# Performance work log

Hardware: AMD Instinct MI355X
Metric: run time of the kernel (lower is better)

## Reference

```python
import jax, jax.numpy as jnp
import numpy as np

NUM_HEADS = 16
HEAD_DIM = 32  # dim=512 / num_heads=16


def _rel_pos_bias(table, index, window_area):
    # table: [(2W-1)^2, H], index: [N, N] int -> bias [1, H, N, N]
    bias = table[index.reshape(-1)].reshape(window_area, window_area, -1)
    return jnp.transpose(bias, (2, 0, 1))[None]


def setup_inputs() -> dict:
    key = jax.random.key(0)
    ks = jax.random.split(key, 6)
    B, N, C = 256, 196, 512
    x = jax.random.normal(ks[0], (B, N, C), dtype=jnp.float32)
    qkv_w = jax.random.normal(ks[1], (3 * C, C), dtype=jnp.float32) * 0.02
    proj_w = jax.random.normal(ks[2], (C, C), dtype=jnp.float32) * 0.02
    proj_b = jax.random.normal(ks[3], (C,), dtype=jnp.float32) * 0.02
    rel_pos_bias_table = jax.random.normal(ks[4], (729, NUM_HEADS), dtype=jnp.float32) * 0.02
    rel_pos_index = jax.random.randint(ks[5], (N, N), 0, 729, dtype=jnp.int64)
    return {
        "x": x,
        "qkv_w": qkv_w,
        "proj_w": proj_w,
        "proj_b": proj_b,
        "rel_pos_bias_table": rel_pos_bias_table,
        "rel_pos_index": rel_pos_index,
        "window_area": N,
    }


def reference(x, qkv_w, proj_w, proj_b, rel_pos_bias_table, rel_pos_index, window_area):
    B, N, C = x.shape
    H, hd = NUM_HEADS, HEAD_DIM
    scale = hd ** -0.5
    # qkv projection (no bias), split into q,k,v: [B, H, N, hd]
    qkv = (x @ qkv_w.T).reshape(B, N, 3, H, hd)
    qkv = jnp.transpose(qkv, (2, 0, 3, 1, 4))
    q, k, v = qkv[0], qkv[1], qkv[2]
    attn = jnp.einsum("bhnd,bhmd->bhnm", q * scale, k)
    attn = attn + _rel_pos_bias(rel_pos_bias_table, rel_pos_index, window_area)
    attn = jax.nn.softmax(attn, axis=-1)
    out = jnp.einsum("bhnm,bhmd->bhnd", attn, v)
    out = jnp.transpose(out, (0, 2, 1, 3)).reshape(B, N, C)
    return out @ proj_w.T + proj_b
```

## Files before the change

### kernel.cpp

```cpp
#include <hip/hip_runtime.h>
#include <hip/hip_bf16.h>


typedef unsigned short u16;
typedef unsigned int u32;
typedef __attribute__((ext_vector_type(8))) short bf16x8;
typedef __attribute__((ext_vector_type(4))) float f32x4;

#define AS1 __attribute__((address_space(1)))
#define AS3 __attribute__((address_space(3)))

__device__ __forceinline__ u16 f2bf(float f) {
  union { float f; unsigned u; } c; c.f = f;
  unsigned r = ((c.u >> 16) & 1u) + 0x7fffu;
  return (u16)((c.u + r) >> 16);
}

__global__ __launch_bounds__(256) void cvt_f32_bf16(const float* __restrict__ in,
                                                    u16* __restrict__ out, int n) {
  int i = (blockIdx.x * 256 + threadIdx.x) * 4;
  if (i >= n) return;
  float4 v = *(const float4*)(in + i);
  ushort4 o;
  o.x = f2bf(v.x); o.y = f2bf(v.y); o.z = f2bf(v.z); o.w = f2bf(v.w);
  *(ushort4*)(out + i) = o;
}

__global__ __launch_bounds__(256) void zero_vt_pad(u16* __restrict__ vt) {
  int i = blockIdx.x * 256 + threadIdx.x;
  if (i >= 4096 * 32 * 36) return;
  int row = i / 36, c = i - row * 36;
  vt[row * 232 + 196 + c] = 0;
}

__global__ __launch_bounds__(256) void build_bias(const float* __restrict__ table,
                                                  const int* __restrict__ idx,
                                                  u16* __restrict__ outb) {
  int e = blockIdx.x * 256 + threadIdx.x;
  int r = e & 3, lane = (e >> 2) & 63, rest = e >> 8;
  int mt = rest % 14; rest /= 14;
  int nt = rest % 13; int h = rest / 13;
  int n = nt * 16 + (lane & 15);
  int m = mt * 16 + ((lane >> 4) << 2) + r;
  float v;
  if (m < 196) {
    int nc = n < 196 ? n : 195;
    v = table[idx[nc * 196 + m] * 16 + h];
  } else {
    v = -1e30f;
  }
  outb[e] = f2bf(v);
}

template<int KT>
__device__ __forceinline__ void ktile(u16* __restrict__ SMEM,
    const u16* __restrict__ gA0, const u16* __restrict__ gA1,
    const u16* __restrict__ gB0, const u16* __restrict__ gB1,
    int wbase, int rdA, int rdB, f32x4 (&acc)[8][4]) {
  constexpr int BUF = KT & 1, OBUF = BUF ^ 1;
  constexpr bool STG = (KT < 7);
  constexpr int C = (KT + 1) * 64;
  bf16x8 afr[4], bfr[4];

#define LOADPAIR(dst, g0, g1, coloff)                                          \
  __builtin_amdgcn_global_load_lds((const AS1 void*)((g0) + (coloff)),         \
      (AS3 void*)&SMEM[(dst) + wbase], 16, 0, 0);                              \
  __builtin_amdgcn_global_load_lds((const AS1 void*)((g1) + (coloff)),         \
      (AS3 void*)&SMEM[(dst) + 4096 + wbase], 16, 0, 0);
#define MFMA16(FH)                                                             \
  __builtin_amdgcn_s_setprio(1);                                               \
  _Pragma("unroll") for (int q = 0; q < 4; ++q)                                \
    _Pragma("unroll") for (int j = 0; j < 4; ++j)                              \
      acc[(FH)*4 + q][j] = __builtin_amdgcn_mfma_f32_16x16x32_bf16(            \
          afr[q], bfr[j], acc[(FH)*4 + q][j], 0, 0, 0);                        \
  __builtin_amdgcn_s_setprio(0);

#pragma unroll
  for (int j = 0; j < 4; ++j) bfr[j] = *(const bf16x8*)&SMEM[rdB + BUF * 16384 + j * 512];
#pragma unroll
  for (int q = 0; q < 4; ++q) afr[q] = *(const bf16x8*)&SMEM[rdA + BUF * 16384 + q * 512];
  if constexpr (STG) { LOADPAIR(OBUF * 16384, gA0, gA1, C) }
  __builtin_amdgcn_s_barrier();
  asm volatile("s_waitcnt lgkmcnt(0)" ::: "memory");
  MFMA16(0)
  __builtin_amdgcn_s_barrier();
#pragma unroll
  for (int q = 0; q < 4; ++q) afr[q] = *(const bf16x8*)&SMEM[rdA + BUF * 16384 + (q + 4) * 512];
  if constexpr (STG) { LOADPAIR(32768 + OBUF * 16384, gB0, gB1, C) }
  __builtin_amdgcn_s_barrier();
  asm volatile("s_waitcnt lgkmcnt(0)" ::: "memory");
  MFMA16(1)
  if constexpr (STG) { asm volatile("s_waitcnt vmcnt(4)" ::: "memory"); }
  else               { asm volatile("s_waitcnt vmcnt(0)" ::: "memory"); }
  __builtin_amdgcn_s_barrier();
#pragma unroll
  for (int j = 0; j < 4; ++j) bfr[j] = *(const bf16x8*)&SMEM[rdB + BUF * 16384 + 8192 + j * 512];
#pragma unroll
  for (int q = 0; q < 4; ++q) afr[q] = *(const bf16x8*)&SMEM[rdA + BUF * 16384 + 8192 + q * 512];
  if constexpr (STG) { LOADPAIR(OBUF * 16384 + 8192, gA0, gA1, C + 32) }
  __builtin_amdgcn_s_barrier();
  asm volatile("s_waitcnt lgkmcnt(0)" ::: "memory");
  MFMA16(0)
  __builtin_amdgcn_s_barrier();
#pragma unroll
  for (int q = 0; q < 4; ++q) afr[q] = *(const bf16x8*)&SMEM[rdA + BUF * 16384 + 8192 + (q + 4) * 512];
  if constexpr (STG) { LOADPAIR(32768 + OBUF * 16384 + 8192, gB0, gB1, C + 32) }
  __builtin_amdgcn_s_barrier();
  asm volatile("s_waitcnt lgkmcnt(0)" ::: "memory");
  MFMA16(1)
  if constexpr (STG) { asm volatile("s_waitcnt vmcnt(4)" ::: "memory"); }
  __builtin_amdgcn_s_barrier();
#undef LOADPAIR
#undef MFMA16
}

template<int EPI>
__global__ __launch_bounds__(512, 2) void gemm8p(
    const u16* __restrict__ A, const u16* __restrict__ Bt,
    u16* __restrict__ q, u16* __restrict__ kk, u16* __restrict__ vt,
    const float* __restrict__ pbias, float* __restrict__ out) {
  constexpr int NWGX = (EPI == 0) ? 6 : 2;
  constexpr int NWG = NWGX * 196;
  __shared__ __align__(16) u16 SMEM[65536];

  int id = blockIdx.y * NWGX + blockIdx.x;
  int nf = (id & 7) * (NWG >> 3) + (id >> 3);
  const int bx = nf / NWGX, by = nf - (nf / NWGX) * NWGX;

  const int tid = threadIdx.x;
  const int w = tid >> 6, l = tid & 63;
  const int lr = l & 15, lg = l >> 4;
  const int wm = w >> 2, wn = w & 3;

  const int gsw = (l & 3) ^ ((l >> 3) & 3);
  const u16* gA0 = A + (size_t)(bx * 256 + w * 16 + (l >> 2)) * 512 + gsw * 8;
  const u16* gA1 = gA0 + 65536;
  const u16* gB0 = Bt + (size_t)(by * 256 + w * 16 + (l >> 2)) * 512 + gsw * 8;
  const u16* gB1 = gB0 + 65536;
  const int wbase = w * 512;

  const int rsw = (lg ^ ((lr >> 1) & 3)) * 8;
  const int rdA = (wm * 128 + lr) * 32 + rsw;
  const int rdB = 32768 + (wn * 64 + lr) * 32 + rsw;

  f32x4 acc[8][4] = {};

#define PLP(dst, g0, g1, coloff)                                               \
  __builtin_amdgcn_global_load_lds((const AS1 void*)((g0) + (coloff)),         \
      (AS3 void*)&SMEM[(dst) + wbase], 16, 0, 0);                              \
  __builtin_amdgcn_global_load_lds((const AS1 void*)((g1) + (coloff)),         \
      (AS3 void*)&SMEM[(dst) + 4096 + wbase], 16, 0, 0);
  PLP(0, gA0, gA1, 0)
  asm volatile("" ::: "memory");
  PLP(32768, gB0, gB1, 0)
  asm volatile("" ::: "memory");
  PLP(8192, gA0, gA1, 32)
  asm volatile("" ::: "memory");
  PLP(32768 + 8192, gB0, gB1, 32)
#undef PLP
  asm volatile("s_waitcnt vmcnt(4)" ::: "memory");
  __builtin_amdgcn_s_barrier();

  ktile<0>(SMEM, gA0, gA1, gB0, gB1, wbase, rdA, rdB, acc);
  ktile<1>(SMEM, gA0, gA1, gB0, gB1, wbase, rdA, rdB, acc);
  ktile<2>(SMEM, gA0, gA1, gB0, gB1, wbase, rdA, rdB, acc);
  ktile<3>(SMEM, gA0, gA1, gB0, gB1, wbase, rdA, rdB, acc);
  ktile<4>(SMEM, gA0, gA1, gB0, gB1, wbase, rdA, rdB, acc);
  ktile<5>(SMEM, gA0, gA1, gB0, gB1, wbase, rdA, rdB, acc);
  ktile<6>(SMEM, gA0, gA1, gB0, gB1, wbase, rdA, rdB, acc);
  ktile<7>(SMEM, gA0, gA1, gB0, gB1, wbase, rdA, rdB, acc);

  if (EPI == 0) {
    const int t = by >> 1;
    const int colbase = by * 256;
    const float s = (t == 0) ? 0.17677669529663687f : 1.0f;
#pragma unroll
    for (int p = 0; p < 2; ++p) {
      __syncthreads();
      if (wm == p) {
        if (t < 2) {
#pragma unroll
        for (int f = 0; f < 8; ++f)
#pragma unroll
          for (int j2 = 0; j2 < 4; ++j2)
#pragma unroll
            for (int r = 0; r < 4; ++r)
              SMEM[(f * 16 + lg * 4 + r) * 264 + wn * 64 + j2 * 16 + lr] =
                  f2bf(acc[f][j2][r] * s);
        } else {
#pragma unroll
        for (int f = 0; f < 8; ++f)
#pragma unroll
          for (int j2 = 0; j2 < 4; ++j2)
#pragma unroll
            for (int r = 0; r < 4; ++r)
              SMEM[(wn * 64 + j2 * 16 + lr) * 136 + f * 16 + lg * 4 + r] =
                  f2bf(acc[f][j2][r]);
        }
      }
      __syncthreads();
      const int growbase = bx * 256 + p * 128;
      if (t < 2) {
        u16* dst = (t == 0) ? q : kk;
        const int lrow = tid >> 2, ch = tid & 3;
        const int grow = growbase + lrow;
        const int bb2 = grow / 196, nn = grow - bb2 * 196;
#pragma unroll
        for (int i = 0; i < 8; ++i) {
          const int colle = (ch + i * 4) * 8;
          bf16x8 vv = *(const bf16x8*)&SMEM[lrow * 264 + colle];
          const int col = colbase + colle;
          const int h = (col >> 5) & 15, dd = col & 31;
          *(bf16x8*)&dst[((size_t)(bb2 * 16 + h) * 196 + nn) * 32 + dd] = vv;
        }
      } else {
        const int cl = tid >> 1, half = tid & 1;
        const int col = colbase + cl;
        const int h = (col >> 5) & 15, dd = col & 31;
#pragma unroll
        for (int i = 0; i < 8; ++i) {
          const int r0 = growbase + half * 64 + i * 8;
          bf16x8 vv = *(const bf16x8*)&SMEM[cl * 136 + half * 64 + i * 8];
          const int bb2 = r0 / 196, nn = r0 - bb2 * 196;
          if (nn + 8 <= 196) {
            *(bf16x8*)&vt[((size_t)(bb2 * 16 + h) * 32 + dd) * 232 + nn] = vv;
          } else {
#pragma unroll
            for (int e = 0; e < 8; ++e) {
              const int rr = r0 + e;
              const int b3 = rr / 196, n3 = rr - b3 * 196;
              vt[((size_t)(b3 * 16 + h) * 32 + dd) * 232 + n3] = (u16)((short*)&vv)[e];
            }
          }
        }
      }
    }
  } else {
    const int colbase = by * 256 + wn * 64;
    const int rowb = bx * 256 + wm * 128 + lg * 4;
#pragma unroll
    for (int f = 0; f < 8; ++f) {
      const int row0 = rowb + f * 16;
#pragma unroll
      for (int j2 = 0; j2 < 4; ++j2) {
        const int col = colbase + j2 * 16 + lr;
        const float pb = pbias[col];
#pragma unroll
        for (int r = 0; r < 4; ++r)
          out[(size_t)(row0 + r) * 512 + col] = acc[f][j2][r] + pb;
      }
    }
  }
}

__global__ __launch_bounds__(256, 4) void attn_kernel(
    const u16* __restrict__ q, const u16* __restrict__ kk,
    const u16* __restrict__ vt, const u16* __restrict__ biasA,
    u16* __restrict__ ao) {
  __shared__ u16 Ks[196 * 40];
  __shared__ u16 Vs[32 * 232];
  const int bhd = blockIdx.x;
  const int h = bhd >> 8, bb = bhd & 255;
  const int bh = bb * 16 + h;
  const int tid = threadIdx.x, w = tid >> 6, l = tid & 63;
  const int lr = l & 15, lg = l >> 4;

  {
    const u16* kg = kk + (size_t)bh * (196 * 32);
#pragma unroll
    for (int p = 0; p < 4; ++p) {
      int m = p * 64 + (tid >> 2);
      if (m < 196) {
        int c = (tid & 3) * 8;
        *(bf16x8*)&Ks[m * 40 + c] = *(const bf16x8*)(kg + m * 32 + c);
      }
    }
    const u16* vg = vt + (size_t)bh * (32 * 232);
#pragma unroll
    for (int p = 0; p < 4; ++p) {
      int off = (p * 256 + tid) * 8;
      if (off < 32 * 232) *(bf16x8*)&Vs[off] = *(const bf16x8*)(vg + off);
    }
  }
  __syncthreads();

  const u16* biasH = biasA + (size_t)h * (13 * 14 * 256);
  const int sA = ((l & 16) << 1) + lr;
  const int sB = sA + 16;
  const bool hi = (l & 32) != 0;

  for (int nt = w; nt < 13; nt += 4) {
    int nq = nt * 16 + lr; if (nq > 195) nq = 195;
    bf16x8 qa = *(const bf16x8*)(q + ((size_t)bh * 196 + nq) * 32 + lg * 8);

    u32 pk[14][2];
    float ssum = 0.f;
#pragma unroll
    for (int mt = 0; mt < 14; ++mt) {
      int row = mt * 16 + lr; if (row > 195) row = 195;
      bf16x8 kb = *(const bf16x8*)&Ks[row * 40 + lg * 8];
      const ushort4 b4 = *(const ushort4*)(biasH + ((nt * 14 + mt) * 64 + l) * 4);
      f32x4 c;
      c[0] = __uint_as_float(((u32)b4.x) << 16);
      c[1] = __uint_as_float(((u32)b4.y) << 16);
      c[2] = __uint_as_float(((u32)b4.z) << 16);
      c[3] = __uint_as_float(((u32)b4.w) << 16);
      f32x4 S = __builtin_amdgcn_mfma_f32_16x16x32_bf16(kb, qa, c, 0, 0, 0);
      float e0 = __expf(S[0]), e1 = __expf(S[1]);
      float e2 = __expf(S[2]), e3 = __expf(S[3]);
      ssum += (e0 + e1) + (e2 + e3);
      asm("v_cvt_pk_bf16_f32 %0, %1, %2" : "=v"(pk[mt][0]) : "v"(e0), "v"(e1));
      asm("v_cvt_pk_bf16_f32 %0, %1, %2" : "=v"(pk[mt][1]) : "v"(e2), "v"(e3));
    }
    ssum += __shfl_xor(ssum, 16);
    ssum += __shfl_xor(ssum, 32);
    float invT = __builtin_amdgcn_rcpf(ssum);

    f32x4 O0 = {}, O1 = {};
#pragma unroll
    for (int ks = 0; ks < 7; ++ks) {
      u32 a0 = (u32)__shfl((int)pk[2 * ks][0], sA);
      u32 a1 = (u32)__shfl((int)pk[2 * ks][1], sA);
      u32 a2 = (u32)__shfl((int)pk[2 * ks][0], sB);
      u32 a3 = (u32)__shfl((int)pk[2 * ks][1], sB);
      u32 c0 = (u32)__shfl((int)pk[2 * ks + 1][0], sA);
      u32 c1 = (u32)__shfl((int)pk[2 * ks + 1][1], sA);
      u32 c2 = (u32)__shfl((int)pk[2 * ks + 1][0], sB);
      u32 c3 = (u32)__shfl((int)pk[2 * ks + 1][1], sB);
      bf16x8 pa;
      ((u32*)&pa)[0] = hi ? c0 : a0;
      ((u32*)&pa)[1] = hi ? c1 : a1;
      ((u32*)&pa)[2] = hi ? c2 : a2;
      ((u32*)&pa)[3] = hi ? c3 : a3;
      bf16x8 v0 = *(const bf16x8*)&Vs[lr * 232 + ks * 32 + lg * 8];
      bf16x8 v1 = *(const bf16x8*)&Vs[(16 + lr) * 232 + ks * 32 + lg * 8];
      O0 = __builtin_amdgcn_mfma_f32_16x16x32_bf16(pa, v0, O0, 0, 0, 0);
      O1 = __builtin_amdgcn_mfma_f32_16x16x32_bf16(pa, v1, O1, 0, 0, 0);
    }

    float inv[4];
#pragma unroll
    for (int r = 0; r < 4; ++r) inv[r] = __shfl(invT, lg * 4 + r);
    const int nr0 = nt * 16 + lg * 4;
#pragma unroll
    for (int r = 0; r < 4; ++r) {
      int nr = nr0 + r;
      if (nr < 196) {
        size_t base = ((size_t)bb * 196 + nr) * 512 + h * 32;
        ao[base + lr] = f2bf(O0[r] * inv[r]);
        ao[base + 16 + lr] = f2bf(O1[r] * inv[r]);
      }
    }
  }
}

extern "C" void kernel_launch(void* const* d_in, const int* in_sizes, int n_in,
                              void* d_out, int out_size, void* d_ws, size_t ws_size,
                              hipStream_t stream) {
  const float* x      = (const float*)d_in[0];
  const float* qkv_w  = (const float*)d_in[1];
  const float* proj_w = (const float*)d_in[2];
  const float* proj_b = (const float*)d_in[3];
  const float* table  = (const float*)d_in[4];
  const int*   ridx   = (const int*)d_in[5];
  float* out = (float*)d_out;

  char* ws = (char*)d_ws;
  u16*   xb    = (u16*)(ws);
  u16*   qwb   = (u16*)(ws + 51380224);
  u16*   pwb   = (u16*)(ws + 52953088);
  u16*   qb    = (u16*)(ws + 53477376);
  u16*   kb    = (u16*)(ws + 104857600);
  u16*   vtb   = (u16*)(ws + 156237824);
  u16*   biasA = (u16*)(ws + 217055232);

  cvt_f32_bf16<<<25088, 256, 0, stream>>>(x, xb, 25690112);
  cvt_f32_bf16<<<768, 256, 0, stream>>>(qkv_w, qwb, 786432);
  cvt_f32_bf16<<<256, 256, 0, stream>>>(proj_w, pwb, 262144);
  build_bias<<<2912, 256, 0, stream>>>(table, ridx, biasA);
  zero_vt_pad<<<18432, 256, 0, stream>>>(vtb);

  gemm8p<0><<<dim3(6, 196), 512, 0, stream>>>(xb, qwb, qb, kb, vtb, nullptr, nullptr);
  attn_kernel<<<4096, 256, 0, stream>>>(qb, kb, vtb, biasA, xb );
  gemm8p<1><<<dim3(2, 196), 512, 0, stream>>>(xb, pwb, nullptr, nullptr, nullptr, proj_b, out);
}
```

Baseline: 273.7 us.

## Hoist K/V fragments into registers, interleave QK and PV, drop pad kernel

The attention kernel now loads all K and V MFMA fragments from shared memory into registers once per block instead of once per query tile. QK^T and PV are interleaved per pair of key tiles, so the 14-entry probability buffer is no longer live. The V padding columns beyond 196 are zeroed in registers, which removes the separate zero_vt_pad launch. Occupancy hint drops from 4 to 3 blocks per SIMD to make room for the larger register footprint, which risks lower latency hiding.

After: 338.5 us. 1.24x slower.

```diff
diff --git a/kernel.cpp b/kernel.cpp
--- a/kernel.cpp
+++ b/kernel.cpp
@@ -24,13 +24,6 @@
   ushort4 o;
   o.x = f2bf(v.x); o.y = f2bf(v.y); o.z = f2bf(v.z); o.w = f2bf(v.w);
   *(ushort4*)(out + i) = o;
-}
-
-__global__ __launch_bounds__(256) void zero_vt_pad(u16* __restrict__ vt) {
-  int i = blockIdx.x * 256 + threadIdx.x;
-  if (i >= 4096 * 32 * 36) return;
-  int row = i / 36, c = i - row * 36;
-  vt[row * 232 + 196 + c] = 0;
 }
 
 __global__ __launch_bounds__(256) void build_bias(const float* __restrict__ table,
@@ -253,7 +246,7 @@
   }
 }
 
-__global__ __launch_bounds__(256, 4) void attn_kernel(
+__global__ __launch_bounds__(256, 3) void attn_kernel(
     const u16* __restrict__ q, const u16* __restrict__ kk,
     const u16* __restrict__ vt, const u16* __restrict__ biasA,
     u16* __restrict__ ao) {
@@ -284,6 +277,27 @@
   }
   __syncthreads();
 
+  bf16x8 kb[14], va[7], vb[7];
+#pragma unroll
+  for (int mt = 0; mt < 14; ++mt) {
+    int row = mt * 16 + lr; if (row > 195) row = 195;
+    kb[mt] = *(const bf16x8*)&Ks[row * 40 + lg * 8];
+  }
+#pragma unroll
+  for (int ks = 0; ks < 7; ++ks) {
+    va[ks] = *(const bf16x8*)&Vs[lr * 232 + ks * 32 + lg * 8];
+    vb[ks] = *(const bf16x8*)&Vs[(16 + lr) * 232 + ks * 32 + lg * 8];
+  }
+  {
+    bf16x8 z = {};
+    if (lg == 0) {
+      va[6][4] = 0; va[6][5] = 0; va[6][6] = 0; va[6][7] = 0;
+      vb[6][4] = 0; vb[6][5] = 0; vb[6][6] = 0; vb[6][7] = 0;
+    } else {
+      va[6] = z; vb[6] = z;
+    }
+  }
+
   const u16* biasH = biasA + (size_t)h * (13 * 14 * 256);
   const int sA = ((l & 16) << 1) + lr;
   const int sB = sA + 16;
@@ -292,51 +306,62 @@
   for (int nt = w; nt < 13; nt += 4) {
     int nq = nt * 16 + lr; if (nq > 195) nq = 195;
     bf16x8 qa = *(const bf16x8*)(q + ((size_t)bh * 196 + nq) * 32 + lg * 8);
-
-    u32 pk[14][2];
     float ssum = 0.f;
-#pragma unroll
-    for (int mt = 0; mt < 14; ++mt) {
-      int row = mt * 16 + lr; if (row > 195) row = 195;
-      bf16x8 kb = *(const bf16x8*)&Ks[row * 40 + lg * 8];
-      const ushort4 b4 = *(const ushort4*)(biasH + ((nt * 14 + mt) * 64 + l) * 4);
-      f32x4 c;
-      c[0] = __uint_as_float(((u32)b4.x) << 16);
-      c[1] = __uint_as_float(((u32)b4.y) << 16);
-      c[2] = __uint_as_float(((u32)b4.z) << 16);
-      c[3] = __uint_as_float(((u32)b4.w) << 16);
-      f32x4 S = __builtin_amdgcn_mfma_f32_16x16x32_bf16(kb, qa, c, 0, 0, 0);
-      float e0 = __expf(S[0]), e1 = __expf(S[1]);
-      float e2 = __expf(S[2]), e3 = __expf(S[3]);
-      ssum += (e0 + e1) + (e2 + e3);
-      asm("v_cvt_pk_bf16_f32 %0, %1, %2" : "=v"(pk[mt][0]) : "v"(e0), "v"(e1));
-      asm("v_cvt_pk_bf16_f32 %0, %1, %2" : "=v"(pk[mt][1]) : "v"(e2), "v"(e3));
-    }
-    ssum += __shfl_xor(ssum, 16);
-    ssum += __shfl_xor(ssum, 32);
-    float invT = __builtin_amdgcn_rcpf(ssum);
-
     f32x4 O0 = {}, O1 = {};
+
 #pragma unroll
     for (int ks = 0; ks < 7; ++ks) {
-      u32 a0 = (u32)__shfl((int)pk[2 * ks][0], sA);
-      u32 a1 = (u32)__shfl((int)pk[2 * ks][1], sA);
-      u32 a2 = (u32)__shfl((int)pk[2 * ks][0], sB);
-      u32 a3 = (u32)__shfl((int)pk[2 * ks][1], sB);
-      u32 c0 = (u32)__shfl((int)pk[2 * ks + 1][0], sA);
-      u32 c1 = (u32)__shfl((int)pk[2 * ks + 1][1], sA);
-      u32 c2 = (u32)__shfl((int)pk[2 * ks + 1][0], sB);
-      u32 c3 = (u32)__shfl((int)pk[2 * ks + 1][1], sB);
+      u32 pk0, pk1, pk2, pk3;
+      {
+        const int mt = 2 * ks;
+        const ushort4 b4 = *(const ushort4*)(biasH + ((nt * 14 + mt) * 64 + l) * 4);
+        f32x4 c;
+        c[0] = __uint_as_float(((u32)b4.x) << 16);
+        c[1] = __uint_as_float(((u32)b4.y) << 16);
+        c[2] = __uint_as_float(((u32)b4.z) << 16);
+        c[3] = __uint_as_float(((u32)b4.w) << 16);
+        f32x4 S = __builtin_amdgcn_mfma_f32_16x16x32_bf16(kb[mt], qa, c, 0, 0, 0);
+        float e0 = __expf(S[0]), e1 = __expf(S[1]);
+        float e2 = __expf(S[2]), e3 = __expf(S[3]);
+        ssum += (e0 + e1) + (e2 + e3);
+        asm("v_cvt_pk_bf16_f32 %0, %1, %2" : "=v"(pk0) : "v"(e0), "v"(e1));
+        asm("v_cvt_pk_bf16_f32 %0, %1, %2" : "=v"(pk1) : "v"(e2), "v"(e3));
+      }
+      {
+        const int mt = 2 * ks + 1;
+        const ushort4 b4 = *(const ushort4*)(biasH + ((nt * 14 + mt) * 64 + l) * 4);
+        f32x4 c;
+        c[0] = __uint_as_float(((u32)b4.x) << 16);
+        c[1] = __uint_as_float(((u32)b4.y) << 16);
+        c[2] = __uint_as_float(((u32)b4.z) << 16);
+        c[3] = __uint_as_float(((u32)b4.w) << 16);
+        f32x4 S = __builtin_amdgcn_mfma_f32_16x16x32_bf16(kb[mt], qa, c, 0, 0, 0);
+        float e0 = __expf(S[0]), e1 = __expf(S[1]);
+        float e2 = __expf(S[2]), e3 = __expf(S[3]);
+        ssum += (e0 + e1) + (e2 + e3);
+        asm("v_cvt_pk_bf16_f32 %0, %1, %2" : "=v"(pk2) : "v"(e0), "v"(e1));
+        asm("v_cvt_pk_bf16_f32 %0, %1, %2" : "=v"(pk3) : "v"(e2), "v"(e3));
+      }
+      u32 a0 = (u32)__shfl((int)pk0, sA);
+      u32 a1 = (u32)__shfl((int)pk1, sA);
+      u32 a2 = (u32)__shfl((int)pk0, sB);
+      u32 a3 = (u32)__shfl((int)pk1, sB);
+      u32 c0 = (u32)__shfl((int)pk2, sA);
+      u32 c1 = (u32)__shfl((int)pk3, sA);
+      u32 c2 = (u32)__shfl((int)pk2, sB);
+      u32 c3 = (u32)__shfl((int)pk3, sB);
       bf16x8 pa;
       ((u32*)&pa)[0] = hi ? c0 : a0;
       ((u32*)&pa)[1] = hi ? c1 : a1;
       ((u32*)&pa)[2] = hi ? c2 : a2;
       ((u32*)&pa)[3] = hi ? c3 : a3;
-      bf16x8 v0 = *(const bf16x8*)&Vs[lr * 232 + ks * 32 + lg * 8];
-      bf16x8 v1 = *(const bf16x8*)&Vs[(16 + lr) * 232 + ks * 32 + lg * 8];
-      O0 = __builtin_amdgcn_mfma_f32_16x16x32_bf16(pa, v0, O0, 0, 0, 0);
-      O1 = __builtin_amdgcn_mfma_f32_16x16x32_bf16(pa, v1, O1, 0, 0, 0);
-    }
+      O0 = __builtin_amdgcn_mfma_f32_16x16x32_bf16(pa, va[ks], O0, 0, 0, 0);
+      O1 = __builtin_amdgcn_mfma_f32_16x16x32_bf16(pa, vb[ks], O1, 0, 0, 0);
+    }
+
+    ssum += __shfl_xor(ssum, 16);
+    ssum += __shfl_xor(ssum, 32);
+    float invT = __builtin_amdgcn_rcpf(ssum);
 
     float inv[4];
 #pragma unroll
@@ -378,7 +403,6 @@
   cvt_f32_bf16<<<768, 256, 0, stream>>>(qkv_w, qwb, 786432);
   cvt_f32_bf16<<<256, 256, 0, stream>>>(proj_w, pwb, 262144);
   build_bias<<<2912, 256, 0, stream>>>(table, ridx, biasA);
-  zero_vt_pad<<<18432, 256, 0, stream>>>(vtb);
 
   gemm8p<0><<<dim3(6, 196), 512, 0, stream>>>(xb, qwb, qb, kb, vtb, nullptr, nullptr);
   attn_kernel<<<4096, 256, 0, stream>>>(qb, kb, vtb, biasA, xb );
```
